# Optimization experiments

Hardware: AMD Instinct MI355X
Metric: run time of the kernel (lower is better)

The kernel has to match this reference:

```python
import jax, jax.numpy as jnp
import numpy as np

K = 12
CHUNK = 1024
N_LAYERS = 4
WIDTH = 192
COND = 64
PE_DIM = 3 * 8 * 2 + 3  # 51
OUT_SCALE = 0.01
BIG = 1e9


def _build_knn(x, k=K, chunk=CHUNK):
    """Brute-force kNN, row-chunked like the TF double-chunked version.
    x: (N,3) float32 -> (N,k) int32 neighbor indices (self excluded)."""
    n = x.shape[0]
    x = x.astype(jnp.float32)
    x_sq = jnp.sum(x * x, axis=1)  # (N,)
    col_ids = jnp.arange(n, dtype=jnp.int32)
    starts = jnp.arange(0, n, chunk, dtype=jnp.int32)

    def one_chunk(start):
        xc = jax.lax.dynamic_slice(x, (start, 0), (chunk, 3))        # (chunk,3)
        sq_c = jax.lax.dynamic_slice(x_sq, (start,), (chunk,))       # (chunk,)
        d = sq_c[:, None] + x_sq[None, :] - 2.0 * (xc @ x.T)         # (chunk,N)
        d = jnp.maximum(d, 0.0)
        rows = start + jnp.arange(chunk, dtype=jnp.int32)
        d = d + jnp.where(rows[:, None] == col_ids[None, :], BIG, 0.0)  # exclude self
        _, idx = jax.lax.top_k(-d, k)                                 # smallest distances
        return idx.astype(jnp.int32)

    idx = jax.lax.map(one_chunk, starts)  # (n/chunk, chunk, k)
    return idx.reshape(n, k)


def _fourier(x, Bs):
    """concat_k [sin(xB_k), cos(xB_k)] + x  -> (N, PE_DIM)."""
    feats = []
    for B in Bs:
        xb = x @ B  # (N,8)
        feats.append(jnp.sin(xb))
        feats.append(jnp.cos(xb))
    feats.append(x)
    return jnp.concatenate(feats, axis=-1)


def setup_inputs() -> dict:
    key = jax.random.key(0)
    ks = jax.random.split(key, 16)
    n = 32768
    x = jax.random.normal(ks[0], (n, 3), dtype=jnp.float32)
    z = jax.random.normal(ks[1], (COND,), dtype=jnp.float32)
    sigmas = (1.0, 10.0, 50.0)
    B0 = jax.random.normal(ks[2], (3, 8), dtype=jnp.float32) * sigmas[0]
    B1 = jax.random.normal(ks[3], (3, 8), dtype=jnp.float32) * sigmas[1]
    B2 = jax.random.normal(ks[4], (3, 8), dtype=jnp.float32) * sigmas[2]
    in_total = PE_DIM + COND  # 115
    s = 0.05
    Wp = jax.random.normal(ks[5], (in_total, WIDTH), dtype=jnp.float32) * s
    bp = jnp.zeros((WIDTH,), dtype=jnp.float32)
    mix_dim = WIDTH + WIDTH + 6  # feat + agg + rel_feat
    Wl = jax.random.normal(ks[6], (N_LAYERS, mix_dim, WIDTH), dtype=jnp.float32) * s
    bl = jnp.zeros((N_LAYERS, WIDTH), dtype=jnp.float32)
    # FiLM: kernel ~zeros, gamma bias=ones, beta bias=zeros (perturbed slightly)
    Wg = jax.random.normal(ks[7], (N_LAYERS, COND, WIDTH), dtype=jnp.float32) * 0.01
    bg = jnp.ones((N_LAYERS, WIDTH), dtype=jnp.float32)
    Wb = jax.random.normal(ks[8], (N_LAYERS, COND, WIDTH), dtype=jnp.float32) * 0.01
    bb = jnp.zeros((N_LAYERS, WIDTH), dtype=jnp.float32)
    Wout = jax.random.normal(ks[9], (WIDTH, 3), dtype=jnp.float32) * s
    bout = jnp.zeros((3,), dtype=jnp.float32)
    return {"x": x, "z": z, "B0": B0, "B1": B1, "B2": B2,
            "Wp": Wp, "bp": bp, "Wl": Wl, "bl": bl,
            "Wg": Wg, "bg": bg, "Wb": Wb, "bb": bb,
            "Wout": Wout, "bout": bout}


def reference(x, z, B0, B1, B2, Wp, bp, Wl, bl, Wg, bg, Wb, bb, Wout, bout):
    n = x.shape[0]
    knn_idx = _build_knn(x)                     # (N,K) int32
    pe = _fourier(x, (B0, B1, B2))              # (N,51)
    zb = jnp.broadcast_to(z[None, :], (n, COND))
    feat = jnp.concatenate([pe, zb], axis=-1)   # (N,115)
    h = jax.nn.silu(feat @ Wp + bp)             # (N,WIDTH)
    # precompute relative-coordinate stats (same for all layers)
    nbr_coords = x[knn_idx]                     # (N,K,3)
    rel = nbr_coords - x[:, None, :]
    rel_feat = jnp.concatenate([rel.mean(axis=1), rel.std(axis=1)], axis=-1)  # (N,6)
    for li in range(N_LAYERS):
        nbr = h[knn_idx]                        # (N,K,WIDTH) gather
        agg = nbr.mean(axis=1)                  # (N,WIDTH)
        mix = jnp.concatenate([h, agg, rel_feat], axis=-1)  # (N,390)
        h = jax.nn.silu(mix @ Wl[li] + bl[li])
        gamma = z @ Wg[li] + bg[li]             # (WIDTH,)
        beta = z @ Wb[li] + bb[li]
        h = h * gamma[None, :] + beta[None, :]  # FiLM
    out = (h @ Wout + bout) * OUT_SCALE         # (N,3)
    return out
```

## Files before the change

kernel.cpp:

```cpp
#include <hip/hip_runtime.h>
#include <math.h>

#define WIDTH 192
#define KNN 12
#define G 64
#define NCELLS (G * G * G)
#define SMAX 8

#define CE(a, b) { double _lo = fmin(a, b); double _hi = fmax(a, b); a = _lo; b = _hi; }
#define INSERT12(key) { \
    b11 = fmin(b11, key); \
    CE(b10, b11); CE(b9, b10); CE(b8, b9); CE(b7, b8); CE(b6, b7); \
    CE(b5, b6);  CE(b4, b5); CE(b3, b4); CE(b2, b3); CE(b1, b2); CE(b0, b1); }
#define DECL12 double b0,b1,b2,b3,b4,b5,b6,b7,b8,b9,b10,b11
#define INIT12 { b0=__hiloint2double(0x7F7FFFFF,0);  b1=__hiloint2double(0x7F7FFFFF,1); \
    b2=__hiloint2double(0x7F7FFFFF,2);  b3=__hiloint2double(0x7F7FFFFF,3); \
    b4=__hiloint2double(0x7F7FFFFF,4);  b5=__hiloint2double(0x7F7FFFFF,5); \
    b6=__hiloint2double(0x7F7FFFFF,6);  b7=__hiloint2double(0x7F7FFFFF,7); \
    b8=__hiloint2double(0x7F7FFFFF,8);  b9=__hiloint2double(0x7F7FFFFF,9); \
    b10=__hiloint2double(0x7F7FFFFF,10); b11=__hiloint2double(0x7F7FFFFF,11); }

#define MERGE_STAGE(m) { \
    double pb11 = shflx_d(b11, m), pb10 = shflx_d(b10, m), pb9 = shflx_d(b9, m); \
    double pb8  = shflx_d(b8, m),  pb7  = shflx_d(b7, m),  pb6 = shflx_d(b6, m); \
    double pb5  = shflx_d(b5, m),  pb4  = shflx_d(b4, m),  pb3 = shflx_d(b3, m); \
    double pb2  = shflx_d(b2, m),  pb1  = shflx_d(b1, m),  pb0 = shflx_d(b0, m); \
    double c12 = pb3, c13 = pb2, c14 = pb1, c15 = pb0; \
    b4 = fmin(b4, pb11); b5 = fmin(b5, pb10); b6 = fmin(b6, pb9);  b7 = fmin(b7, pb8); \
    b8 = fmin(b8, pb7);  b9 = fmin(b9, pb6);  b10 = fmin(b10, pb5); b11 = fmin(b11, pb4); \
    CE(b0, b8);  CE(b1, b9);  CE(b2, b10); CE(b3, b11); \
    CE(b4, c12); CE(b5, c13); CE(b6, c14); CE(b7, c15); \
    CE(b0, b4);  CE(b1, b5);  CE(b2, b6);  CE(b3, b7); \
    CE(b8, c12); CE(b9, c13); CE(b10, c14); CE(b11, c15); \
    CE(b0, b2);  CE(b1, b3);  CE(b4, b6);  CE(b5, b7); \
    CE(b8, b10); CE(b9, b11); \
    CE(b0, b1);  CE(b2, b3);  CE(b4, b5);  CE(b6, b7); \
    CE(b8, b9);  CE(b10, b11); }

__device__ inline unsigned encf(float f) {
    unsigned u = __float_as_uint(f);
    return (u & 0x80000000u) ? ~u : (u | 0x80000000u);
}
__device__ inline float decf(unsigned u) {
    return (u & 0x80000000u) ? __uint_as_float(u & 0x7fffffffu) : __uint_as_float(~u);
}
__device__ inline int cellc(float v, float mn, float invh) {
    int c = (int)((v - mn) * invh);
    return min(max(c, 0), G - 1);
}
__device__ inline double shflx_d(double v, int m) {
    int lo = __shfl_xor(__double2loint(v), m, 64);
    int hi = __shfl_xor(__double2hiint(v), m, 64);
    return __hiloint2double(hi, lo);
}

__device__ inline float wave_union_d12(
    double b0, double b1, double b2, double b3, double b4, double b5,
    double b6, double b7, double b8, double b9, double b10, double b11)
{
#pragma unroll
    for (int m = 1; m <= 32; m <<= 1) MERGE_STAGE(m)
    return __int_as_float(__double2hiint(b11));
}

__global__ __launch_bounds__(256) void prep_kernel(
    const float4* __restrict__ sorted, const float* __restrict__ B0,
    const float* __restrict__ B1, const float* __restrict__ B2,
    float* __restrict__ pe, int n)
{
    int i = blockIdx.x * 256 + threadIdx.x;
    float4 q = sorted[i];
    float x0 = q.x, x1 = q.y, x2 = q.z;
    const float* Bm[3] = {B0, B1, B2};
    float* pr = pe + (size_t)i * 64;
#pragma unroll
    for (int m = 0; m < 3; ++m) {
        const float* B = Bm[m];
#pragma unroll
        for (int k = 0; k < 8; ++k) {
            float arg = x0 * B[k] + x1 * B[8 + k] + x2 * B[16 + k];
            pr[m * 16 + k]     = sinf(arg);
            pr[m * 16 + 8 + k] = cosf(arg);
        }
    }
    pr[48] = x0; pr[49] = x1; pr[50] = x2;
#pragma unroll
    for (int c = 51; c < 64; ++c) pr[c] = 0.0f;
}

__global__ __launch_bounds__(256) void precompute_kernel(
    const float* __restrict__ z, const float* __restrict__ Wp, const float* __restrict__ bp,
    const float* __restrict__ Wg, const float* __restrict__ bg,
    const float* __restrict__ Wb, const float* __restrict__ bb,
    float* __restrict__ bias0, float* __restrict__ gammaB, float* __restrict__ betaB)
{
    __shared__ float zs[64];
    int t = threadIdx.x;
    if (t < 64) zs[t] = z[t];
    __syncthreads();
    if (t < WIDTH) {
        float acc = bp[t];
        for (int k = 0; k < 64; ++k) acc += zs[k] * Wp[(51 + k) * WIDTH + t];
        bias0[t] = acc;
        for (int l = 0; l < 4; ++l) {
            float g = bg[l * WIDTH + t];
            float b = bb[l * WIDTH + t];
            for (int k = 0; k < 64; ++k) {
                g += zs[k] * Wg[(l * 64 + k) * WIDTH + t];
                b += zs[k] * Wb[(l * 64 + k) * WIDTH + t];
            }
            gammaB[l * WIDTH + t] = g;
            betaB[l * WIDTH + t] = b;
        }
    }
}

__global__ __launch_bounds__(64) void init_bbox_kernel(unsigned* __restrict__ bb)
{
    int t = threadIdx.x;
    if (t < 3) bb[t] = 0xFFFFFFFFu;
    else if (t < 6) bb[t] = 0u;
}

__global__ __launch_bounds__(256) void bbox_kernel(
    const float* __restrict__ x, unsigned* __restrict__ bb, int n)
{
    int i = blockIdx.x * 256 + threadIdx.x;
    unsigned emin[3], emax[3];
#pragma unroll
    for (int a = 0; a < 3; ++a) { unsigned e = encf(x[i * 3 + a]); emin[a] = e; emax[a] = e; }
#pragma unroll
    for (int o = 32; o; o >>= 1) {
#pragma unroll
        for (int a = 0; a < 3; ++a) {
            emin[a] = min(emin[a], (unsigned)__shfl_xor((int)emin[a], o, 64));
            emax[a] = max(emax[a], (unsigned)__shfl_xor((int)emax[a], o, 64));
        }
    }
    if ((threadIdx.x & 63) == 0) {
#pragma unroll
        for (int a = 0; a < 3; ++a) {
            atomicMin(&bb[a], emin[a]);
            atomicMax(&bb[3 + a], emax[a]);
        }
    }
}

__global__ __launch_bounds__(256) void hist_kernel(
    const float* __restrict__ x, const unsigned* __restrict__ bb,
    unsigned* __restrict__ counts, unsigned long long* __restrict__ rowmask, int n)
{
    int i = blockIdx.x * 256 + threadIdx.x;
    float mnx = decf(bb[0]), mny = decf(bb[1]), mnz = decf(bb[2]);
    float ivx = (float)G / (decf(bb[3]) - mnx);
    float ivy = (float)G / (decf(bb[4]) - mny);
    float ivz = (float)G / (decf(bb[5]) - mnz);
    int cx = cellc(x[i * 3 + 0], mnx, ivx);
    int cy = cellc(x[i * 3 + 1], mny, ivy);
    int cz = cellc(x[i * 3 + 2], mnz, ivz);
    atomicAdd(&counts[(cz * G + cy) * G + cx], 1u);
    atomicOr(&rowmask[cz * G + cy], 1ull << cx);
}

__global__ __launch_bounds__(256) void scan1_kernel(
    const unsigned* __restrict__ counts, unsigned* __restrict__ offs,
    unsigned* __restrict__ bsums)
{
    __shared__ unsigned s[256];
    int b = blockIdx.x, t = threadIdx.x;
    unsigned base = (unsigned)b * 1024 + t * 4;
    unsigned v[4], sum = 0;
#pragma unroll
    for (int k = 0; k < 4; ++k) { v[k] = counts[base + k]; sum += v[k]; }
    s[t] = sum; __syncthreads();
    for (int off = 1; off < 256; off <<= 1) {
        unsigned xv = (t >= off) ? s[t - off] : 0u;
        __syncthreads();
        s[t] += xv;
        __syncthreads();
    }
    unsigned excl = s[t] - sum;
    if (t == 255) bsums[b] = s[255];
    unsigned run = excl;
#pragma unroll
    for (int k = 0; k < 4; ++k) { offs[base + k] = run; run += v[k]; }
}

__global__ __launch_bounds__(256) void scan2_kernel(unsigned* __restrict__ bsums)
{
    __shared__ unsigned s[256];
    int t = threadIdx.x;
    unsigned v = bsums[t];
    s[t] = v; __syncthreads();
    for (int off = 1; off < 256; off <<= 1) {
        unsigned xv = (t >= off) ? s[t - off] : 0u;
        __syncthreads();
        s[t] += xv;
        __syncthreads();
    }
    bsums[t] = s[t] - v;
}

__global__ __launch_bounds__(256) void scan3_kernel(
    unsigned* __restrict__ offs, const unsigned* __restrict__ bsums,
    unsigned* __restrict__ cursors, int n)
{
    int b = blockIdx.x, t = threadIdx.x;
    unsigned add = bsums[b];
    unsigned base = (unsigned)b * 1024 + t * 4;
#pragma unroll
    for (int k = 0; k < 4; ++k) {
        unsigned v = offs[base + k] + add;
        offs[base + k] = v;
        cursors[base + k] = v;
    }
    if (b == 255 && t == 255) offs[NCELLS] = (unsigned)n;
}

__global__ __launch_bounds__(256) void scatter_kernel(
    const float* __restrict__ x, const unsigned* __restrict__ bb,
    unsigned* __restrict__ cursors, float4* __restrict__ sorted,
    unsigned* __restrict__ inv, int n)
{
    int i = blockIdx.x * 256 + threadIdx.x;
    float mnx = decf(bb[0]), mny = decf(bb[1]), mnz = decf(bb[2]);
    float ivx = (float)G / (decf(bb[3]) - mnx);
    float ivy = (float)G / (decf(bb[4]) - mny);
    float ivz = (float)G / (decf(bb[5]) - mnz);
    float x0 = x[i * 3 + 0], x1 = x[i * 3 + 1], x2 = x[i * 3 + 2];
    int cx = cellc(x0, mnx, ivx);
    int cy = cellc(x1, mny, ivy);
    int cz = cellc(x2, mnz, ivz);
    unsigned pos = atomicAdd(&cursors[(cz * G + cy) * G + cx], 1u);
    sorted[pos] = make_float4(x0, x1, x2, __int_as_float(i));
    inv[i] = pos;
}

__global__ __launch_bounds__(64) void knn_grid_kernel(
    const float4* __restrict__ sorted, const unsigned* __restrict__ offs,
    const unsigned long long* __restrict__ rowmask,
    const unsigned* __restrict__ bb, const float* __restrict__ x,
    const unsigned* __restrict__ inv,
    unsigned short* __restrict__ knn, float* __restrict__ relf, int n)
{
    const int l = threadIdx.x;
    const int b = blockIdx.x;
    const int nch = gridDim.x >> 6;
    const int ch = b >> 6, pos = b & 63;
    const int fch = (ch & 1) ? (nch - 1 - (ch >> 1)) : (ch >> 1);
    const int p = fch * 64 + pos;

    float mnx = decf(bb[0]), mny = decf(bb[1]), mnz = decf(bb[2]);
    float mxx = decf(bb[3]), mxy = decf(bb[4]), mxz = decf(bb[5]);
    float hx = (mxx - mnx) / G, hy = (mxy - mny) / G, hz = (mxz - mnz) / G;
    float ivx = (float)G / (mxx - mnx);
    float ivy = (float)G / (mxy - mny);
    float ivz = (float)G / (mxz - mnz);

    float4 q = sorted[p];
    float xi = q.x, yi = q.y, zi = q.z;
    int iorig = __float_as_int(q.w);
    float sqi = fmaf(zi, zi, fmaf(yi, yi, xi * xi));
    int cx = cellc(xi, mnx, ivx), cy = cellc(yi, mny, ivy), cz = cellc(zi, mnz, ivz);
    float fx = (xi - mnx) - cx * hx;
    float fy = (yi - mny) - cy * hy;
    float fz = (zi - mnz) - cz * hz;

    DECL12; INIT12;
    float worst = 3.402823466e+38f;
    float worst_g = 3.402823466e+38f;
    int nc = 0;
    bool have12 = false;

    auto waveMinWorst = [&]() -> float {
        float wm = worst;
        wm = fminf(wm, __shfl_xor(wm, 1, 64));
        wm = fminf(wm, __shfl_xor(wm, 2, 64));
        wm = fminf(wm, __shfl_xor(wm, 4, 64));
        wm = fminf(wm, __shfl_xor(wm, 8, 64));
        wm = fminf(wm, __shfl_xor(wm, 16, 64));
        wm = fminf(wm, __shfl_xor(wm, 32, 64));
        return wm;
    };

    auto lane12Bound = [&]() -> float {
        float v = __int_as_float(__double2hiint(b0));
#pragma unroll
        for (int k = 2; k <= 64; k <<= 1) {
#pragma unroll
            for (int j = k >> 1; j >= 1; j >>= 1) {
                float pv = __shfl_xor(v, j, 64);
                bool dir = ((l & k) == 0);
                bool lower = ((l & j) == 0);
                float mn = fminf(v, pv), mx = fmaxf(v, pv);
                v = (lower == dir) ? mn : mx;
            }
        }
        return __shfl(v, 11, 64);
    };

    auto scanRange = [&](int c0, int c1) {
        unsigned j0 = offs[c0], j1 = offs[c1 + 1];
        if (j0 >= j1) return;
        float4 c = sorted[j0];
        for (unsigned t = j0; t < j1; ++t) {
            unsigned tn = (t + 1 < j1) ? t + 1 : t;
            float4 nx = sorted[tn];
            float sqj = fmaf(c.z, c.z, fmaf(c.y, c.y, c.x * c.x));
            float dot = fmaf(zi, c.z, fmaf(yi, c.y, xi * c.x));
            float d = fmaf(-2.0f, dot, sqi + sqj);
            int jg = __float_as_int(c.w);
            if (d <= fminf(worst, worst_g) && jg != iorig) {
                d = fmaxf(d, 0.0f);
                double key = __hiloint2double(__float_as_int(d), jg);
                INSERT12(key);
                worst = __int_as_float(__double2hiint(b11));
                ++nc;
            }
            c = nx;
        }
    };

    auto scanStrided = [&](int c0, int c1, int sub, int step) {
        unsigned j0 = offs[c0], j1 = offs[c1 + 1];
        for (unsigned t = j0 + sub; t < j1; t += step) {
            float4 c = sorted[t];
            float sqj = fmaf(c.z, c.z, fmaf(c.y, c.y, c.x * c.x));
            float dot = fmaf(zi, c.z, fmaf(yi, c.y, xi * c.x));
            float d = fmaf(-2.0f, dot, sqi + sqj);
            int jg = __float_as_int(c.w);
            if (d <= fminf(worst, worst_g) && jg != iorig) {
                d = fmaxf(d, 0.0f);
                double key = __hiloint2double(__float_as_int(d), jg);
                INSERT12(key);
                worst = __int_as_float(__double2hiint(b11));
                ++nc;
            }
        }
    };

    auto doRow = [&](int s, int dz, int dy, int sub, int step) {
        int zz = cz + dz, yy = cy + dy;
        if (zz < 0 || zz >= G || yy < 0 || yy >= G) return;
        int row = zz * G + yy;
        unsigned long long rm = rowmask[row];
        if (rm == 0ull) return;
        int rb = row * G;
        int adz = dz < 0 ? -dz : dz, ady = dy < 0 ? -dy : dy;
        if (adz == s || ady == s) {
            int x0 = max(cx - s, 0), x1 = min(cx + s, G - 1);
            unsigned long long msk =
                ((x1 == 63) ? ~0ull : ((1ull << (x1 + 1)) - 1ull)) &
                ~((1ull << x0) - 1ull);
            unsigned long long mm = rm & msk;
            if (mm) {
                int c0 = __ffsll((unsigned long long)mm) - 1;
                int c1 = 63 - __clzll((long long)mm);
                if (step == 1) scanRange(rb + c0, rb + c1);
                else           scanStrided(rb + c0, rb + c1, sub, step);
            }
        } else {
            int xm = cx - s, xp = cx + s;
            if (xm >= 0 && ((rm >> xm) & 1ull)) {
                if (step == 1) scanRange(rb + xm, rb + xm);
                else           scanStrided(rb + xm, rb + xm, sub, step);
            }
            if (xp < G && ((rm >> xp) & 1ull)) {
                if (step == 1) scanRange(rb + xp, rb + xp);
                else           scanStrided(rb + xp, rb + xp, sub, step);
            }
        }
    };

    auto check12 = [&]() {
        if (!have12) {
            int ns = nc;
#pragma unroll
            for (int o = 1; o <= 32; o <<= 1) ns += __shfl_xor(ns, o, 64);
            have12 = (ns >= 12);
        }
    };

    bool done = false;
    for (int s = 0; s <= SMAX; ++s) {
        if (s > 0) {
            float bx = (s - 1) * hx + fminf(fx, hx - fx);
            float by = (s - 1) * hy + fminf(fy, hy - fy);
            float bz = (s - 1) * hz + fminf(fz, hz - fz);
            float bnd = fminf(bx, fminf(by, bz));
            float bnd2 = bnd * bnd;
            worst_g = fminf(worst_g, waveMinWorst());
            if (bnd2 > worst_g + 1e-4f) { done = true; break; }
            unsigned long long anyb =
                __ballot(__double2hiint(b0) != 0x7F7FFFFF);
            if (__popcll(anyb) >= 12) {
                worst_g = fminf(worst_g, lane12Bound());
                if (bnd2 > worst_g + 1e-4f) { done = true; break; }
            }
            if (s >= 2) {
                check12();
                if (have12) {
                    worst_g = fminf(worst_g,
                        wave_union_d12(b0,b1,b2,b3,b4,b5,b6,b7,b8,b9,b10,b11));
                    if (bnd2 > worst_g + 1e-4f) { done = true; break; }
                }
            }
        }
        if (s == 0) {
            int row = cz * G + cy;
            if ((rowmask[row] >> cx) & 1ull) {
                int rb = row * G;
                scanStrided(rb + cx, rb + cx, l, 64);
            }
        } else {
            int w2 = 2 * s + 1;
            int nrows = w2 * w2;
            int lpr = 64 / nrows;
            if (lpr > 1) {
                int r = l / lpr, sub = l - r * lpr;
                if (r < nrows) {
                    int dz = r / w2 - s, dy = r - (r / w2) * w2 - s;
                    doRow(s, dz, dy, sub, lpr);
                }
            } else {
                float rcp = 1.0f / (float)w2;
                for (int r = l; r < nrows; r += 64) {
                    int qd = (int)((float)r * rcp);
                    int rem = r - qd * w2;
                    if (rem < 0) { qd--; rem += w2; }
                    else if (rem >= w2) { qd++; rem -= w2; }
                    doRow(s, qd - s, rem - s, 0, 1);
                }
            }
        }
    }
    if (!done) {
        float bx = SMAX * hx + fminf(fx, hx - fx);
        float by = SMAX * hy + fminf(fy, hy - fy);
        float bz = SMAX * hz + fminf(fz, hz - fz);
        float bnd = fminf(bx, fminf(by, bz));
        float bnd2 = bnd * bnd;
        worst_g = fminf(worst_g, waveMinWorst());
        if (bnd2 > worst_g + 1e-4f) done = true;
        if (!done) {
            unsigned long long anyb =
                __ballot(__double2hiint(b0) != 0x7F7FFFFF);
            if (__popcll(anyb) >= 12) {
                worst_g = fminf(worst_g, lane12Bound());
                if (bnd2 > worst_g + 1e-4f) done = true;
            }
        }
        if (!done) {
            check12();
            if (have12) {
                worst_g = fminf(worst_g,
                    wave_union_d12(b0,b1,b2,b3,b4,b5,b6,b7,b8,b9,b10,b11));
                if (bnd2 > worst_g + 1e-4f) done = true;
            }
        }
    }
    if (!done) {
        INIT12;
        worst = 3.402823466e+38f;
        for (int base = 0; base < n; base += 512) {
            float4 cc[8];
#pragma unroll
            for (int r = 0; r < 8; ++r) cc[r] = sorted[base + l + r * 64];
#pragma unroll
            for (int r = 0; r < 8; ++r) {
                float4 c = cc[r];
                float sqj = fmaf(c.z, c.z, fmaf(c.y, c.y, c.x * c.x));
                float dot = fmaf(zi, c.z, fmaf(yi, c.y, xi * c.x));
                float d = fmaf(-2.0f, dot, sqi + sqj);
                int jg = __float_as_int(c.w);
                if (d <= fminf(worst, worst_g) && jg != iorig) {
                    d = fmaxf(d, 0.0f);
                    double key = __hiloint2double(__float_as_int(d), jg);
                    INSERT12(key);
                    worst = __int_as_float(__double2hiint(b11));
                }
            }
        }
    }

#pragma unroll
    for (int m = 1; m <= 32; m <<= 1) MERGE_STAGE(m)

    if (l == 0) {
        int idx[KNN];
        idx[0]=__double2loint(b0);  idx[1]=__double2loint(b1);  idx[2]=__double2loint(b2);
        idx[3]=__double2loint(b3);  idx[4]=__double2loint(b4);  idx[5]=__double2loint(b5);
        idx[6]=__double2loint(b6);  idx[7]=__double2loint(b7);  idx[8]=__double2loint(b8);
        idx[9]=__double2loint(b9);  idx[10]=__double2loint(b10); idx[11]=__double2loint(b11);

        float rx[KNN], ry[KNN], rz[KNN];
        float sx = 0.f, sy = 0.f, sz = 0.f;
#pragma unroll
        for (int s = 0; s < KNN; ++s) {
            int j = idx[s];
            knn[(size_t)p * KNN + s] = (unsigned short)inv[j];
            rx[s] = x[(size_t)j * 3 + 0] - xi;
            ry[s] = x[(size_t)j * 3 + 1] - yi;
            rz[s] = x[(size_t)j * 3 + 2] - zi;
            sx += rx[s]; sy += ry[s]; sz += rz[s];
        }
        float mx = sx / 12.0f, my = sy / 12.0f, mz = sz / 12.0f;
        float vx = 0.f, vy = 0.f, vz = 0.f;
#pragma unroll
        for (int s = 0; s < KNN; ++s) {
            float dx = rx[s] - mx, dy = ry[s] - my, dz = rz[s] - mz;
            vx += dx * dx; vy += dy * dy; vz += dz * dz;
        }
        float* rr = relf + (size_t)p * 8;
        rr[0] = mx; rr[1] = my; rr[2] = mz;
        rr[3] = sqrtf(vx / 12.0f); rr[4] = sqrtf(vy / 12.0f); rr[5] = sqrtf(vz / 12.0f);
        rr[6] = 0.0f; rr[7] = 0.0f;
    }
}

template <bool LAYER>
__global__ __launch_bounds__(256) void gemm_silu_kernel(
    const float* __restrict__ A0, const unsigned short* __restrict__ knnp,
    const float* __restrict__ Rel,
    const float* __restrict__ W, const float* __restrict__ bias,
    const float* __restrict__ gamma, const float* __restrict__ beta,
    float* __restrict__ out)
{
    __shared__ float As[16][68];
    __shared__ float Bs[16][196];
    const int tid = threadIdx.x;
    const int ty = tid >> 4, tx = tid & 15;
    const int m0 = blockIdx.x * 64;
    const int arow = tid >> 2, akoff = (tid & 3) * 4;
    const int bk = tid >> 4,  bc = (tid & 15) * 12;

    float acc[4][12] = {};
    const int NCH = LAYER ? 24 : 4;

    unsigned kf[6] = {0, 0, 0, 0, 0, 0};
    if (LAYER) {
        const unsigned* kp = (const unsigned*)(knnp + (size_t)(m0 + arow) * KNN);
#pragma unroll
        for (int w = 0; w < 6; ++w) kf[w] = kp[w];
    }

    auto loadA = [&](int ch) -> float4 {
        int k0 = ch * 16;
        if (!LAYER) {
            return *(const float4*)&A0[(size_t)(m0 + arow) * 64 + k0 + akoff];
        } else if (k0 < 192) {
            return *(const float4*)&A0[(size_t)(m0 + arow) * 192 + k0 + akoff];
        } else {
            int c4 = (k0 - 192 + akoff) >> 2;
            const float4* h4 = (const float4*)A0;
            float4 s = make_float4(0.f, 0.f, 0.f, 0.f);
#pragma unroll
            for (int j = 0; j < KNN; ++j) {
                unsigned idx = (j & 1) ? (kf[j >> 1] >> 16) : (kf[j >> 1] & 0xFFFFu);
                float4 v = h4[(size_t)idx * 48 + c4];
                s.x += v.x; s.y += v.y; s.z += v.z; s.w += v.w;
            }
            const float r = 1.0f / 12.0f;
            return make_float4(s.x * r, s.y * r, s.z * r, s.w * r);
        }
    };

    float4 ra = loadA(0);
    const float* wr0 = &W[(size_t)bk * 192 + bc];
    float4 rb0 = *(const float4*)&wr0[0];
    float4 rb1 = *(const float4*)&wr0[4];
    float4 rb2 = *(const float4*)&wr0[8];

    for (int ch = 0; ch < NCH; ++ch) {
        As[akoff + 0][arow] = ra.x; As[akoff + 1][arow] = ra.y;
        As[akoff + 2][arow] = ra.z; As[akoff + 3][arow] = ra.w;
        *(float4*)&Bs[bk][bc + 0] = rb0;
        *(float4*)&Bs[bk][bc + 4] = rb1;
        *(float4*)&Bs[bk][bc + 8] = rb2;
        __syncthreads();
        if (ch + 1 < NCH) {
            ra = loadA(ch + 1);
            const float* wr = &W[(size_t)((ch + 1) * 16 + bk) * 192 + bc];
            rb0 = *(const float4*)&wr[0];
            rb1 = *(const float4*)&wr[4];
            rb2 = *(const float4*)&wr[8];
        }
#pragma unroll
        for (int k = 0; k < 16; ++k) {
            float4 a0 = *(const float4*)&As[k][ty * 4];
            float av[4] = {a0.x, a0.y, a0.z, a0.w};
            float4 q0 = *(const float4*)&Bs[k][tx * 12 + 0];
            float4 q1 = *(const float4*)&Bs[k][tx * 12 + 4];
            float4 q2 = *(const float4*)&Bs[k][tx * 12 + 8];
            float bv[12] = {q0.x, q0.y, q0.z, q0.w, q1.x, q1.y, q1.z, q1.w,
                            q2.x, q2.y, q2.z, q2.w};
#pragma unroll
            for (int a = 0; a < 4; ++a)
#pragma unroll
                for (int bcol = 0; bcol < 12; ++bcol)
                    acc[a][bcol] = fmaf(av[a], bv[bcol], acc[a][bcol]);
        }
        __syncthreads();
    }

    if (LAYER) {
        {
            int row = tid >> 2, cp = (tid & 3) * 2;
            float2 v = *(const float2*)&Rel[(size_t)(m0 + row) * 8 + cp];
            As[cp + 0][row] = v.x; As[cp + 1][row] = v.y;
        }
        {
            int k2 = tid >> 4, c = (tid & 15) * 12;
            if (k2 < 8) {
                int gk = 384 + k2; if (gk > 389) gk = 389;
                const float* wr = &W[(size_t)gk * 192 + c];
                *(float4*)&Bs[k2][c + 0] = *(const float4*)&wr[0];
                *(float4*)&Bs[k2][c + 4] = *(const float4*)&wr[4];
                *(float4*)&Bs[k2][c + 8] = *(const float4*)&wr[8];
            }
        }
        __syncthreads();
#pragma unroll
        for (int k = 0; k < 8; ++k) {
            float4 a0 = *(const float4*)&As[k][ty * 4];
            float av[4] = {a0.x, a0.y, a0.z, a0.w};
            float4 q0 = *(const float4*)&Bs[k][tx * 12 + 0];
            float4 q1 = *(const float4*)&Bs[k][tx * 12 + 4];
            float4 q2 = *(const float4*)&Bs[k][tx * 12 + 8];
            float bv[12] = {q0.x, q0.y, q0.z, q0.w, q1.x, q1.y, q1.z, q1.w,
                            q2.x, q2.y, q2.z, q2.w};
#pragma unroll
            for (int a = 0; a < 4; ++a)
#pragma unroll
                for (int bcol = 0; bcol < 12; ++bcol)
                    acc[a][bcol] = fmaf(av[a], bv[bcol], acc[a][bcol]);
        }
        __syncthreads();
    }

#pragma unroll
    for (int a = 0; a < 4; ++a) {
        int gi = m0 + ty * 4 + a;
        float res[12];
#pragma unroll
        for (int bcol = 0; bcol < 12; ++bcol) {
            int gc = tx * 12 + bcol;
            float v = acc[a][bcol] + bias[gc];
            float s = 1.0f / (1.0f + expf(-v));
            v = v * s;
            if (LAYER) v = v * gamma[gc] + beta[gc];
            res[bcol] = v;
        }
        float* orow = &out[(size_t)gi * 192 + tx * 12];
        *(float4*)&orow[0] = make_float4(res[0], res[1], res[2], res[3]);
        *(float4*)&orow[4] = make_float4(res[4], res[5], res[6], res[7]);
        *(float4*)&orow[8] = make_float4(res[8], res[9], res[10], res[11]);
    }
}

__global__ __launch_bounds__(256) void out_kernel(
    const float4* __restrict__ h4, const float4* __restrict__ sorted,
    const float* __restrict__ Wout, const float* __restrict__ bout,
    float* __restrict__ out, int n)
{
    __shared__ float w[576];
    int t = threadIdx.x;
    for (int e = t; e < 576; e += 256) w[e] = Wout[e];
    __syncthreads();
    int i = blockIdx.x * 256 + t;
    float a0 = 0.f, a1 = 0.f, a2 = 0.f;
    for (int k4 = 0; k4 < 48; ++k4) {
        float4 hv = h4[(size_t)i * 48 + k4];
        int k = k4 * 4;
        a0 = fmaf(hv.x, w[k * 3 + 0], a0); a1 = fmaf(hv.x, w[k * 3 + 1], a1); a2 = fmaf(hv.x, w[k * 3 + 2], a2);
        a0 = fmaf(hv.y, w[k * 3 + 3], a0); a1 = fmaf(hv.y, w[k * 3 + 4], a1); a2 = fmaf(hv.y, w[k * 3 + 5], a2);
        a0 = fmaf(hv.z, w[k * 3 + 6], a0); a1 = fmaf(hv.z, w[k * 3 + 7], a1); a2 = fmaf(hv.z, w[k * 3 + 8], a2);
        a0 = fmaf(hv.w, w[k * 3 + 9], a0); a1 = fmaf(hv.w, w[k * 3 + 10], a1); a2 = fmaf(hv.w, w[k * 3 + 11], a2);
    }
    int iorig = __float_as_int(sorted[i].w);
    out[(size_t)iorig * 3 + 0] = (a0 + bout[0]) * 0.01f;
    out[(size_t)iorig * 3 + 1] = (a1 + bout[1]) * 0.01f;
    out[(size_t)iorig * 3 + 2] = (a2 + bout[2]) * 0.01f;
}

extern "C" void kernel_launch(void* const* d_in, const int* in_sizes, int n_in,
                              void* d_out, int out_size, void* d_ws, size_t ws_size,
                              hipStream_t stream)
{
    const float* x    = (const float*)d_in[0];
    const float* z    = (const float*)d_in[1];
    const float* B0   = (const float*)d_in[2];
    const float* B1   = (const float*)d_in[3];
    const float* B2   = (const float*)d_in[4];
    const float* Wp   = (const float*)d_in[5];
    const float* bp   = (const float*)d_in[6];
    const float* Wl   = (const float*)d_in[7];
    const float* bl   = (const float*)d_in[8];
    const float* Wg   = (const float*)d_in[9];
    const float* bg   = (const float*)d_in[10];
    const float* Wb   = (const float*)d_in[11];
    const float* bb   = (const float*)d_in[12];
    const float* Wout = (const float*)d_in[13];
    const float* bout = (const float*)d_in[14];

    int n = in_sizes[0] / 3;

    float* ws = (float*)d_ws;
    float* bias0  = ws;
    float* gammaB = ws + 192;
    float* betaB  = ws + 960;
    size_t off = 1728;
    unsigned short* knn = (unsigned short*)(ws + off);  off += (size_t)n * 6;
    float* relf = ws + off;                off += (size_t)n * 8;
    float4* sorted = (float4*)(ws + off);  off += (size_t)n * 4;
    float* hA   = ws + off;                off += (size_t)n * 192;
    float* hB   = ws + off;                off += (size_t)n * 192;

    unsigned* bbx     = (unsigned*)hA;
    unsigned* counts  = bbx + 8;
    unsigned* offsA   = counts + NCELLS;
    unsigned* cursors = offsA + NCELLS + 1;
    unsigned* bsums   = cursors + NCELLS;
    size_t gu = 8 + (size_t)NCELLS * 3 + 1 + 256;
    gu = (gu + 1) & ~(size_t)1;
    unsigned long long* rowmask = (unsigned long long*)((unsigned*)hA + gu);
    gu += (size_t)G * G * 2;
    unsigned* inv = (unsigned*)hA + gu;
    float* pe = hB;

    init_bbox_kernel<<<1, 64, 0, stream>>>(bbx);
    hipMemsetAsync(counts, 0, (size_t)NCELLS * 4, stream);
    hipMemsetAsync(rowmask, 0, (size_t)G * G * 8, stream);
    precompute_kernel<<<1, 256, 0, stream>>>(z, Wp, bp, Wg, bg, Wb, bb,
                                             bias0, gammaB, betaB);
    bbox_kernel<<<n / 256, 256, 0, stream>>>(x, bbx, n);
    hist_kernel<<<n / 256, 256, 0, stream>>>(x, bbx, counts, rowmask, n);
    scan1_kernel<<<NCELLS / 1024, 256, 0, stream>>>(counts, offsA, bsums);
    scan2_kernel<<<1, 256, 0, stream>>>(bsums);
    scan3_kernel<<<NCELLS / 1024, 256, 0, stream>>>(offsA, bsums, cursors, n);
    scatter_kernel<<<n / 256, 256, 0, stream>>>(x, bbx, cursors, sorted, inv, n);
    prep_kernel<<<n / 256, 256, 0, stream>>>(sorted, B0, B1, B2, pe, n);
    knn_grid_kernel<<<n, 64, 0, stream>>>(sorted, offsA, rowmask, bbx, x,
                                          inv, knn, relf, n);

    gemm_silu_kernel<false><<<n / 64, 256, 0, stream>>>(
        pe, nullptr, nullptr, Wp, bias0, nullptr, nullptr, hA);

    float* hcur = hA;
    float* hnxt = hB;
    for (int li = 0; li < 4; ++li) {
        gemm_silu_kernel<true><<<n / 64, 256, 0, stream>>>(
            hcur, knn, relf,
            Wl + (size_t)li * 390 * 192, bl + (size_t)li * 192,
            gammaB + (size_t)li * 192, betaB + (size_t)li * 192, hnxt);
        float* t = hcur; hcur = hnxt; hnxt = t;
    }

    out_kernel<<<n / 256, 256, 0, stream>>>((const float4*)hcur, sorted,
                                            Wout, bout, (float*)d_out, n);
}
```

Measured before the change: 713.5 us.

## Prune kNN grid rows and cells by distance bound; pack two queries per block

The kNN grid search now computes a lower bound on the squared distance from the query to each candidate row and to each shell cell, and skips rows or cells whose bound exceeds the current 12th-best distance. On shell rows it also narrows the x-range of scanned cells using that bound. Separately, each block now holds two 64-lane wavefronts handling two query points, which halves the block count. The pruning saves distance evaluations and memory reads, at the cost of extra float math per row and some risk of slight bound errors, which the small epsilon is meant to cover.

```diff
diff --git a/kernel.cpp b/kernel.cpp
--- a/kernel.cpp
+++ b/kernel.cpp
@@ -236,19 +236,21 @@
     inv[i] = pos;
 }
 
-__global__ __launch_bounds__(64) void knn_grid_kernel(
+__global__ __launch_bounds__(128) void knn_grid_kernel(
     const float4* __restrict__ sorted, const unsigned* __restrict__ offs,
     const unsigned long long* __restrict__ rowmask,
     const unsigned* __restrict__ bb, const float* __restrict__ x,
     const unsigned* __restrict__ inv,
     unsigned short* __restrict__ knn, float* __restrict__ relf, int n)
 {
-    const int l = threadIdx.x;
+    const int tid = threadIdx.x;
+    const int l = tid & 63;
+    const int w = tid >> 6;
     const int b = blockIdx.x;
-    const int nch = gridDim.x >> 6;
-    const int ch = b >> 6, pos = b & 63;
+    const int nch = n >> 6;
+    const int ch = b >> 5, posb = b & 31;
     const int fch = (ch & 1) ? (nch - 1 - (ch >> 1)) : (ch >> 1);
-    const int p = fch * 64 + pos;
+    const int p = fch * 64 + posb * 2 + w;
 
     float mnx = decf(bb[0]), mny = decf(bb[1]), mnz = decf(bb[2]);
     float mxx = decf(bb[3]), mxy = decf(bb[4]), mxz = decf(bb[5]);
@@ -342,13 +344,21 @@
     auto doRow = [&](int s, int dz, int dy, int sub, int step) {
         int zz = cz + dz, yy = cy + dy;
         if (zz < 0 || zz >= G || yy < 0 || yy >= G) return;
+        int adz = dz < 0 ? -dz : dz, ady = dy < 0 ? -dy : dy;
+        float dzd = (adz > 0) ? ((adz - 1) * hz + ((dz > 0) ? (hz - fz) : fz)) : 0.0f;
+        float dyd = (ady > 0) ? ((ady - 1) * hy + ((dy > 0) ? (hy - fy) : fy)) : 0.0f;
+        float rowmin2 = fmaf(dzd, dzd, dyd * dyd);
+        float wg = fminf(worst, worst_g) + 1e-4f;
+        if (rowmin2 > wg) return;
         int row = zz * G + yy;
         unsigned long long rm = rowmask[row];
         if (rm == 0ull) return;
         int rb = row * G;
-        int adz = dz < 0 ? -dz : dz, ady = dy < 0 ? -dy : dy;
         if (adz == s || ady == s) {
-            int x0 = max(cx - s, 0), x1 = min(cx + s, G - 1);
+            float sqb = sqrtf(wg - rowmin2);
+            int dxp = (int)fminf(fmaxf((sqb - (hx - fx)) / hx + 1.001f, 0.0f), (float)s);
+            int dxm = (int)fminf(fmaxf((sqb - fx) / hx + 1.001f, 0.0f), (float)s);
+            int x0 = max(cx - dxm, 0), x1 = min(cx + dxp, G - 1);
             unsigned long long msk =
                 ((x1 == 63) ? ~0ull : ((1ull << (x1 + 1)) - 1ull)) &
                 ~((1ull << x0) - 1ull);
@@ -361,11 +371,15 @@
             }
         } else {
             int xm = cx - s, xp = cx + s;
-            if (xm >= 0 && ((rm >> xm) & 1ull)) {
+            float dxmd = (s - 1) * hx + fx;
+            float dxpd = (s - 1) * hx + (hx - fx);
+            if (xm >= 0 && ((rm >> xm) & 1ull) &&
+                fmaf(dxmd, dxmd, rowmin2) <= wg) {
                 if (step == 1) scanRange(rb + xm, rb + xm);
                 else           scanStrided(rb + xm, rb + xm, sub, step);
             }
-            if (xp < G && ((rm >> xp) & 1ull)) {
+            if (xp < G && ((rm >> xp) & 1ull) &&
+                fmaf(dxpd, dxpd, rowmin2) <= wg) {
                 if (step == 1) scanRange(rb + xp, rb + xp);
                 else           scanStrided(rb + xp, rb + xp, sub, step);
             }
@@ -740,8 +754,8 @@
     scan3_kernel<<<NCELLS / 1024, 256, 0, stream>>>(offsA, bsums, cursors, n);
     scatter_kernel<<<n / 256, 256, 0, stream>>>(x, bbx, cursors, sorted, inv, n);
     prep_kernel<<<n / 256, 256, 0, stream>>>(sorted, B0, B1, B2, pe, n);
-    knn_grid_kernel<<<n, 64, 0, stream>>>(sorted, offsA, rowmask, bbx, x,
-                                          inv, knn, relf, n);
+    knn_grid_kernel<<<n / 2, 128, 0, stream>>>(sorted, offsA, rowmask, bbx, x,
+                                               inv, knn, relf, n);
 
     gemm_silu_kernel<false><<<n / 64, 256, 0, stream>>>(
         pe, nullptr, nullptr, Wp, bias0, nullptr, nullptr, hA);
```

New measurement: 759.4 us. +6.4%, slower.

## Process two query points per wavefront using 32-lane half-wave groups in kNN

Applied to the files above, without the earlier changes.

The grid kNN kernel now assigns two query points per 64-lane wavefront, one per 32-lane half, and launches half as many blocks. All reductions, bitonic bounds, merges, ballot counts and cell-scan striding are narrowed to 32 lanes, so idle lanes in the sparse shell search carry useful work. The cost is that each query has half the lanes for scanning, and divergent termination between the two halves can keep one half waiting on the other.

```diff
diff --git a/kernel.cpp b/kernel.cpp
--- a/kernel.cpp
+++ b/kernel.cpp
@@ -54,15 +54,6 @@
     return __hiloint2double(hi, lo);
 }
 
-__device__ inline float wave_union_d12(
-    double b0, double b1, double b2, double b3, double b4, double b5,
-    double b6, double b7, double b8, double b9, double b10, double b11)
-{
-#pragma unroll
-    for (int m = 1; m <= 32; m <<= 1) MERGE_STAGE(m)
-    return __int_as_float(__double2hiint(b11));
-}
-
 __global__ __launch_bounds__(256) void prep_kernel(
     const float4* __restrict__ sorted, const float* __restrict__ B0,
     const float* __restrict__ B1, const float* __restrict__ B2,
@@ -244,11 +235,13 @@
     unsigned short* __restrict__ knn, float* __restrict__ relf, int n)
 {
     const int l = threadIdx.x;
+    const int l32 = l & 31;
+    const int g32 = l >> 5;
     const int b = blockIdx.x;
-    const int nch = gridDim.x >> 6;
-    const int ch = b >> 6, pos = b & 63;
+    const int nch = n >> 6;
+    const int ch = b >> 5, posb = b & 31;
     const int fch = (ch & 1) ? (nch - 1 - (ch >> 1)) : (ch >> 1);
-    const int p = fch * 64 + pos;
+    const int p = fch * 64 + posb * 2 + g32;
 
     float mnx = decf(bb[0]), mny = decf(bb[1]), mnz = decf(bb[2]);
     float mxx = decf(bb[3]), mxy = decf(bb[4]), mxz = decf(bb[5]);
@@ -272,31 +265,40 @@
     int nc = 0;
     bool have12 = false;
 
-    auto waveMinWorst = [&]() -> float {
+    auto groupMinWorst = [&]() -> float {
         float wm = worst;
         wm = fminf(wm, __shfl_xor(wm, 1, 64));
         wm = fminf(wm, __shfl_xor(wm, 2, 64));
         wm = fminf(wm, __shfl_xor(wm, 4, 64));
         wm = fminf(wm, __shfl_xor(wm, 8, 64));
         wm = fminf(wm, __shfl_xor(wm, 16, 64));
-        wm = fminf(wm, __shfl_xor(wm, 32, 64));
         return wm;
     };
 
     auto lane12Bound = [&]() -> float {
         float v = __int_as_float(__double2hiint(b0));
 #pragma unroll
-        for (int k = 2; k <= 64; k <<= 1) {
+        for (int k = 2; k <= 32; k <<= 1) {
 #pragma unroll
             for (int j = k >> 1; j >= 1; j >>= 1) {
                 float pv = __shfl_xor(v, j, 64);
-                bool dir = ((l & k) == 0);
-                bool lower = ((l & j) == 0);
+                bool dir = ((l32 & k) == 0);
+                bool lower = ((l32 & j) == 0);
                 float mn = fminf(v, pv), mx = fmaxf(v, pv);
                 v = (lower == dir) ? mn : mx;
             }
         }
-        return __shfl(v, 11, 64);
+        return __shfl(v, (l & 32) | 11, 64);
+    };
+
+    auto groupUnionD12 = [&]() -> float {
+        double c0=b0,c1=b1,c2=b2,c3=b3,c4=b4,c5=b5,c6=b6,c7=b7,c8=b8,c9=b9,c10=b10,c11=b11;
+        {
+            double b0=c0,b1=c1,b2=c2,b3=c3,b4=c4,b5=c5,b6=c6,b7=c7,b8=c8,b9=c9,b10=c10,b11=c11;
+#pragma unroll
+            for (int m = 1; m <= 16; m <<= 1) MERGE_STAGE(m)
+            return __int_as_float(__double2hiint(b11));
+        }
     };
 
     auto scanRange = [&](int c0, int c1) {
@@ -376,7 +378,7 @@
         if (!have12) {
             int ns = nc;
 #pragma unroll
-            for (int o = 1; o <= 32; o <<= 1) ns += __shfl_xor(ns, o, 64);
+            for (int o = 1; o <= 16; o <<= 1) ns += __shfl_xor(ns, o, 64);
             have12 = (ns >= 12);
         }
     };
@@ -389,19 +391,19 @@
             float bz = (s - 1) * hz + fminf(fz, hz - fz);
             float bnd = fminf(bx, fminf(by, bz));
             float bnd2 = bnd * bnd;
-            worst_g = fminf(worst_g, waveMinWorst());
+            worst_g = fminf(worst_g, groupMinWorst());
             if (bnd2 > worst_g + 1e-4f) { done = true; break; }
             unsigned long long anyb =
                 __ballot(__double2hiint(b0) != 0x7F7FFFFF);
-            if (__popcll(anyb) >= 12) {
+            unsigned gm = (unsigned)(anyb >> (g32 << 5));
+            if (__popc(gm) >= 12) {
                 worst_g = fminf(worst_g, lane12Bound());
                 if (bnd2 > worst_g + 1e-4f) { done = true; break; }
             }
             if (s >= 2) {
                 check12();
                 if (have12) {
-                    worst_g = fminf(worst_g,
-                        wave_union_d12(b0,b1,b2,b3,b4,b5,b6,b7,b8,b9,b10,b11));
+                    worst_g = fminf(worst_g, groupUnionD12());
                     if (bnd2 > worst_g + 1e-4f) { done = true; break; }
                 }
             }
@@ -410,21 +412,21 @@
             int row = cz * G + cy;
             if ((rowmask[row] >> cx) & 1ull) {
                 int rb = row * G;
-                scanStrided(rb + cx, rb + cx, l, 64);
+                scanStrided(rb + cx, rb + cx, l32, 32);
             }
         } else {
             int w2 = 2 * s + 1;
             int nrows = w2 * w2;
-            int lpr = 64 / nrows;
+            int lpr = 32 / nrows;
             if (lpr > 1) {
-                int r = l / lpr, sub = l - r * lpr;
+                int r = l32 / lpr, sub = l32 - r * lpr;
                 if (r < nrows) {
                     int dz = r / w2 - s, dy = r - (r / w2) * w2 - s;
                     doRow(s, dz, dy, sub, lpr);
                 }
             } else {
                 float rcp = 1.0f / (float)w2;
-                for (int r = l; r < nrows; r += 64) {
+                for (int r = l32; r < nrows; r += 32) {
                     int qd = (int)((float)r * rcp);
                     int rem = r - qd * w2;
                     if (rem < 0) { qd--; rem += w2; }
@@ -440,12 +442,13 @@
         float bz = SMAX * hz + fminf(fz, hz - fz);
         float bnd = fminf(bx, fminf(by, bz));
         float bnd2 = bnd * bnd;
-        worst_g = fminf(worst_g, waveMinWorst());
+        worst_g = fminf(worst_g, groupMinWorst());
         if (bnd2 > worst_g + 1e-4f) done = true;
         if (!done) {
             unsigned long long anyb =
                 __ballot(__double2hiint(b0) != 0x7F7FFFFF);
-            if (__popcll(anyb) >= 12) {
+            unsigned gm = (unsigned)(anyb >> (g32 << 5));
+            if (__popc(gm) >= 12) {
                 worst_g = fminf(worst_g, lane12Bound());
                 if (bnd2 > worst_g + 1e-4f) done = true;
             }
@@ -453,8 +456,7 @@
         if (!done) {
             check12();
             if (have12) {
-                worst_g = fminf(worst_g,
-                    wave_union_d12(b0,b1,b2,b3,b4,b5,b6,b7,b8,b9,b10,b11));
+                worst_g = fminf(worst_g, groupUnionD12());
                 if (bnd2 > worst_g + 1e-4f) done = true;
             }
         }
@@ -462,10 +464,10 @@
     if (!done) {
         INIT12;
         worst = 3.402823466e+38f;
-        for (int base = 0; base < n; base += 512) {
+        for (int base = 0; base < n; base += 256) {
             float4 cc[8];
 #pragma unroll
-            for (int r = 0; r < 8; ++r) cc[r] = sorted[base + l + r * 64];
+            for (int r = 0; r < 8; ++r) cc[r] = sorted[base + l32 + r * 32];
 #pragma unroll
             for (int r = 0; r < 8; ++r) {
                 float4 c = cc[r];
@@ -484,9 +486,9 @@
     }
 
 #pragma unroll
-    for (int m = 1; m <= 32; m <<= 1) MERGE_STAGE(m)
-
-    if (l == 0) {
+    for (int m = 1; m <= 16; m <<= 1) MERGE_STAGE(m)
+
+    if (l32 == 0) {
         int idx[KNN];
         idx[0]=__double2loint(b0);  idx[1]=__double2loint(b1);  idx[2]=__double2loint(b2);
         idx[3]=__double2loint(b3);  idx[4]=__double2loint(b4);  idx[5]=__double2loint(b5);
@@ -740,8 +742,8 @@
     scan3_kernel<<<NCELLS / 1024, 256, 0, stream>>>(offsA, bsums, cursors, n);
     scatter_kernel<<<n / 256, 256, 0, stream>>>(x, bbx, cursors, sorted, inv, n);
     prep_kernel<<<n / 256, 256, 0, stream>>>(sorted, B0, B1, B2, pe, n);
-    knn_grid_kernel<<<n, 64, 0, stream>>>(sorted, offsA, rowmask, bbx, x,
-                                          inv, knn, relf, n);
+    knn_grid_kernel<<<n / 2, 64, 0, stream>>>(sorted, offsA, rowmask, bbx, x,
+                                              inv, knn, relf, n);
 
     gemm_silu_kernel<false><<<n / 64, 256, 0, stream>>>(
         pe, nullptr, nullptr, Wp, bias0, nullptr, nullptr, hA);
```

New measurement: 740.0 us. +3.7%, slower.
